# Optimization experiments

Hardware: AMD Instinct MI355X
Metric: run time of the kernel (lower is better)

Reference implementation:

```python
import jax, jax.numpy as jnp
import numpy as np

RESOLUTION = 0.1  # init arg `resolution`; hard=True -> hardtanh branch


def setup_inputs() -> dict:
    key = jax.random.key(0)
    B, L = 32, 1024  # documents x sentences per document
    score = jax.random.normal(key, (B * L,), dtype=jnp.float32)
    score_idx = jnp.arange(B * L, dtype=jnp.int32).reshape(B, L)
    return {"score": score, "score_idx": score_idx}


def _toeplitz(s):
    # Equivalent of pad_score: rows i = n-1 .. 1 of concat(zeros(n), s)
    # score_hat[r, j] = s[j - 1 - r] if j - 1 - r >= 0 else 0
    n = s.shape[0]
    r = jnp.arange(n - 1)[:, None]
    j = jnp.arange(n)[None, :]
    idx = j - 1 - r
    return jnp.where(idx >= 0, s[jnp.clip(idx, 0)], jnp.zeros((), s.dtype))


def _prob(score_hat, s):
    # hard=True: (hardtanh((hat - s)/res * 2 + 1) + 1) / 2
    z = (score_hat - s[None, :]) / RESOLUTION * 2.0 + 1.0
    return (jnp.clip(z, -1.0, 1.0) + 1.0) * 0.5


def _gate(s_doc):
    s = s_doc[1:-1]  # drop first/last sentence scores, length n = L-2
    fwd = jnp.cumprod(_prob(_toeplitz(s), s), axis=0)   # [n-1, n]
    sb = s[::-1]
    bwd = jnp.cumprod(_prob(_toeplitz(sb), sb), axis=0)  # [n-1, n]
    return jnp.stack([fwd, bwd], axis=0)  # [2, n-1, n]


def reference(score, score_idx):
    docs = score[score_idx]          # [B, L] gather per score_idx
    return jax.vmap(_gate)(docs)     # [B, 2, L-3, L-2]
```

## Files before the change

### kernel.cpp

```cpp
#include <hip/hip_runtime.h>

#define TPB     256
#define LSEQ    1024
#define NCOL    1022
#define NROW    1021
#define NPAD    1024
#define SLDS    2048
#define NCHUNK  4
#define RPC     256

typedef float v2f __attribute__((ext_vector_type(2)));
typedef float v4f __attribute__((ext_vector_type(4)));

__device__ __forceinline__ float clamp01(float x) {
    return fminf(fmaxf(x, 0.0f), 1.0f);
}

__global__ __launch_bounds__(TPB) void gate_kernel(
    const float* __restrict__ score,
    const int*   __restrict__ score_idx,
    float*       __restrict__ out)
{
    __shared__ __align__(16) float sp[SLDS];

    const int bid = blockIdx.x;
    const int ch  = bid >> 6;
    const int bd  = bid & 63;
    const int d   = bd & 1;
    const int b   = bd >> 1;
    const int tid = threadIdx.x;

    for (int i = tid; i < NPAD; i += TPB) sp[i] = 0.0f;
    if (tid < 2) sp[NPAD + NCOL + tid] = 0.0f;
    const int* idxRow = score_idx + b * LSEQ + 1;
    for (int i = tid; i < NCOL; i += TPB) {
        int src = d ? (NCOL - 1 - i) : i;
        sp[NPAD + i] = score[idxRow[src]];
    }
    __syncthreads();

    const int j = tid * 4;
    const float s0 = sp[NPAD + j    ], s1 = sp[NPAD + j + 1];
    const float s2 = sp[NPAD + j + 2], s3 = sp[NPAD + j + 3];
    const float c0 = 1.0f - 10.0f * s0, c1 = 1.0f - 10.0f * s1;
    const float c2 = 1.0f - 10.0f * s2, c3 = 1.0f - 10.0f * s3;

    float a0 = 1.0f, a1 = 1.0f, a2 = 1.0f, a3 = 1.0f;
    float C1 = s0, C2 = s1, C3 = s2;
    int   m  = NPAD + j - 1;

#define STEP(X)                                                     \
    {   float _x = (X);                                             \
        float p0 = clamp01(__builtin_fmaf(_x, 10.0f, c0));          \
        float p1 = clamp01(__builtin_fmaf(C1, 10.0f, c1));          \
        float p2 = clamp01(__builtin_fmaf(C2, 10.0f, c2));          \
        float p3 = clamp01(__builtin_fmaf(C3, 10.0f, c3));          \
        a0 *= p0; a1 *= p1; a2 *= p2; a3 *= p3;                     \
        C3 = C2; C2 = C1; C1 = _x; }

    #pragma unroll 1
    for (int bt = 0; bt < ch * (RPC / 8); ++bt) {
        v4f hi = *(const v4f*)&sp[m - 3];
        v4f lo = *(const v4f*)&sp[m - 7];
        m -= 8;
        STEP(hi.w); STEP(hi.z); STEP(hi.y); STEP(hi.x);
        STEP(lo.w); STEP(lo.z); STEP(lo.y); STEP(lo.x);
    }

    const int r0 = ch * RPC;
    const int r1 = (r0 + RPC < NROW) ? (r0 + RPC) : NROW;
    const int nrows = r1 - r0;
    const bool half = (tid == TPB - 1);

    float* outp = out + (size_t)bd * NROW * NCOL + (size_t)r0 * NCOL + j;

#define EMIT                                                        \
    {   if (half) { v2f w2; w2.x = a0; w2.y = a1;                   \
                    *(v2f*)outp = w2; }                             \
        else      { v4f w; w.x = a0; w.y = a1; w.z = a2; w.w = a3;  \
                    *(v4f*)outp = w; }                              \
        outp += NCOL; }

    #pragma unroll 1
    for (int bt = 0; bt < nrows / 8; ++bt) {
        v4f hi = *(const v4f*)&sp[m - 3];
        v4f lo = *(const v4f*)&sp[m - 7];
        m -= 8;
        STEP(hi.w); EMIT; STEP(hi.z); EMIT; STEP(hi.y); EMIT; STEP(hi.x); EMIT;
        STEP(lo.w); EMIT; STEP(lo.z); EMIT; STEP(lo.y); EMIT; STEP(lo.x); EMIT;
    }
    #pragma unroll 1
    for (int r = nrows & ~7; r < nrows; ++r) {
        float x = sp[m]; --m;
        STEP(x); EMIT;
    }
#undef STEP
#undef EMIT
}

extern "C" void kernel_launch(void* const* d_in, const int* in_sizes, int n_in,
                              void* d_out, int out_size, void* d_ws, size_t ws_size,
                              hipStream_t stream)
{
    const float* score = (const float*)d_in[0];
    const int*   sidx  = (const int*)d_in[1];
    float*       out   = (float*)d_out;

    const int B = in_sizes[0] / LSEQ;
    dim3 grid(B * 2 * NCHUNK), block(TPB);
    gate_kernel<<<grid, block, 0, stream>>>(score, sidx, out);
}
```

Before: 44.55 us.

## Split row chunks further and precompute chunk prefix products in workspace

Raises the chunk count from 4 to 8 and adds a first kernel that computes each chunk's partial cumulative product, so the store kernel combines earlier chunks' partials instead of replaying all preceding rows serially. This removes the load imbalance where later chunks spent most of their time on prefix recomputation and gives twice as many blocks for the memory-bound store phase. In exchange there is an extra kernel launch plus a small workspace write and read. If the workspace is too small, it falls back to serial recomputation.

```diff
diff --git a/kernel.cpp b/kernel.cpp
--- a/kernel.cpp
+++ b/kernel.cpp
@@ -6,8 +6,10 @@
 #define NROW    1021
 #define NPAD    1024
 #define SLDS    2048
-#define NCHUNK  4
-#define RPC     256
+#define NCHUNK  8
+#define RPC     128
+#define WS_STRIDE 1024
+#define WS_NEED  ((NCHUNK - 1) * 64 * WS_STRIDE * sizeof(float))
 
 typedef float v2f __attribute__((ext_vector_type(2)));
 typedef float v4f __attribute__((ext_vector_type(4)));
@@ -16,20 +18,8 @@
     return fminf(fmaxf(x, 0.0f), 1.0f);
 }
 
-__global__ __launch_bounds__(TPB) void gate_kernel(
-    const float* __restrict__ score,
-    const int*   __restrict__ score_idx,
-    float*       __restrict__ out)
-{
-    __shared__ __align__(16) float sp[SLDS];
-
-    const int bid = blockIdx.x;
-    const int ch  = bid >> 6;
-    const int bd  = bid & 63;
-    const int d   = bd & 1;
-    const int b   = bd >> 1;
-    const int tid = threadIdx.x;
-
+__device__ __forceinline__ void stage(float* sp, const float* score,
+                                      const int* score_idx, int b, int d, int tid) {
     for (int i = tid; i < NPAD; i += TPB) sp[i] = 0.0f;
     if (tid < 2) sp[NPAD + NCOL + tid] = 0.0f;
     const int* idxRow = score_idx + b * LSEQ + 1;
@@ -38,16 +28,7 @@
         sp[NPAD + i] = score[idxRow[src]];
     }
     __syncthreads();
-
-    const int j = tid * 4;
-    const float s0 = sp[NPAD + j    ], s1 = sp[NPAD + j + 1];
-    const float s2 = sp[NPAD + j + 2], s3 = sp[NPAD + j + 3];
-    const float c0 = 1.0f - 10.0f * s0, c1 = 1.0f - 10.0f * s1;
-    const float c2 = 1.0f - 10.0f * s2, c3 = 1.0f - 10.0f * s3;
-
-    float a0 = 1.0f, a1 = 1.0f, a2 = 1.0f, a3 = 1.0f;
-    float C1 = s0, C2 = s1, C3 = s2;
-    int   m  = NPAD + j - 1;
+}
 
 #define STEP(X)                                                     \
     {   float _x = (X);                                             \
@@ -58,25 +39,91 @@
         a0 *= p0; a1 *= p1; a2 *= p2; a3 *= p3;                     \
         C3 = C2; C2 = C1; C1 = _x; }
 
+__global__ __launch_bounds__(TPB) void gate_partial(
+    const float* __restrict__ score,
+    const int*   __restrict__ score_idx,
+    float*       __restrict__ ws)
+{
+    __shared__ __align__(16) float sp[SLDS];
+    const int bid = blockIdx.x;
+    const int c   = bid >> 6;
+    const int bd  = bid & 63;
+    stage(sp, score, score_idx, bd >> 1, bd & 1, threadIdx.x);
+
+    const int j  = threadIdx.x * 4;
+    const int r0 = c * RPC;
+    const float c0 = 1.0f - 10.0f * sp[NPAD + j    ];
+    const float c1 = 1.0f - 10.0f * sp[NPAD + j + 1];
+    const float c2 = 1.0f - 10.0f * sp[NPAD + j + 2];
+    const float c3 = 1.0f - 10.0f * sp[NPAD + j + 3];
+
+    float a0 = 1.0f, a1 = 1.0f, a2 = 1.0f, a3 = 1.0f;
+    float C1 = sp[NPAD + j - r0], C2 = sp[NPAD + j + 1 - r0], C3 = sp[NPAD + j + 2 - r0];
+    int   m  = NPAD + j - 1 - r0;
+
     #pragma unroll 1
-    for (int bt = 0; bt < ch * (RPC / 8); ++bt) {
+    for (int bt = 0; bt < RPC / 8; ++bt) {
         v4f hi = *(const v4f*)&sp[m - 3];
         v4f lo = *(const v4f*)&sp[m - 7];
         m -= 8;
         STEP(hi.w); STEP(hi.z); STEP(hi.y); STEP(hi.x);
         STEP(lo.w); STEP(lo.z); STEP(lo.y); STEP(lo.x);
     }
+    v4f P; P.x = a0; P.y = a1; P.z = a2; P.w = a3;
+    *(v4f*)&ws[(size_t)bid * WS_STRIDE + j] = P;
+}
 
-    const int r0 = ch * RPC;
-    const int r1 = (r0 + RPC < NROW) ? (r0 + RPC) : NROW;
-    const int nrows = r1 - r0;
+template <bool USE_WS>
+__global__ __launch_bounds__(TPB) void gate_store(
+    const float* __restrict__ score,
+    const int*   __restrict__ score_idx,
+    const float* __restrict__ ws,
+    float*       __restrict__ out)
+{
+    __shared__ __align__(16) float sp[SLDS];
+    const int bid = blockIdx.x;
+    const int ch  = bid >> 6;
+    const int bd  = bid & 63;
+    stage(sp, score, score_idx, bd >> 1, bd & 1, threadIdx.x);
+
+    const int tid = threadIdx.x;
+    const int j   = tid * 4;
+    const int r0  = ch * RPC;
+    const float c0 = 1.0f - 10.0f * sp[NPAD + j    ];
+    const float c1 = 1.0f - 10.0f * sp[NPAD + j + 1];
+    const float c2 = 1.0f - 10.0f * sp[NPAD + j + 2];
+    const float c3 = 1.0f - 10.0f * sp[NPAD + j + 3];
+
+    float a0 = 1.0f, a1 = 1.0f, a2 = 1.0f, a3 = 1.0f;
+    float C1, C2, C3;
+    int   m;
+
+    if (USE_WS) {
+        for (int c = 0; c < ch; ++c) {
+            v4f P = *(const v4f*)&ws[(size_t)(c * 64 + bd) * WS_STRIDE + j];
+            a0 *= P.x; a1 *= P.y; a2 *= P.z; a3 *= P.w;
+        }
+        C1 = sp[NPAD + j - r0]; C2 = sp[NPAD + j + 1 - r0]; C3 = sp[NPAD + j + 2 - r0];
+        m  = NPAD + j - 1 - r0;
+    } else {
+        C1 = sp[NPAD + j]; C2 = sp[NPAD + j + 1]; C3 = sp[NPAD + j + 2];
+        m  = NPAD + j - 1;
+        #pragma unroll 1
+        for (int bt = 0; bt < (r0 >> 3); ++bt) {
+            v4f hi = *(const v4f*)&sp[m - 3];
+            v4f lo = *(const v4f*)&sp[m - 7];
+            m -= 8;
+            STEP(hi.w); STEP(hi.z); STEP(hi.y); STEP(hi.x);
+            STEP(lo.w); STEP(lo.z); STEP(lo.y); STEP(lo.x);
+        }
+    }
+
+    const int nrows = (r0 + RPC < NROW) ? RPC : (NROW - r0);
     const bool half = (tid == TPB - 1);
-
     float* outp = out + (size_t)bd * NROW * NCOL + (size_t)r0 * NCOL + j;
 
 #define EMIT                                                        \
-    {   if (half) { v2f w2; w2.x = a0; w2.y = a1;                   \
-                    *(v2f*)outp = w2; }                             \
+    {   if (half) { v2f w2; w2.x = a0; w2.y = a1; *(v2f*)outp = w2; } \
         else      { v4f w; w.x = a0; w.y = a1; w.z = a2; w.w = a3;  \
                     *(v4f*)outp = w; }                              \
         outp += NCOL; }
@@ -94,7 +141,6 @@
         float x = sp[m]; --m;
         STEP(x); EMIT;
     }
-#undef STEP
 #undef EMIT
 }
 
@@ -105,8 +151,12 @@
     const float* score = (const float*)d_in[0];
     const int*   sidx  = (const int*)d_in[1];
     float*       out   = (float*)d_out;
+    float*       ws    = (float*)d_ws;
 
-    const int B = in_sizes[0] / LSEQ;
-    dim3 grid(B * 2 * NCHUNK), block(TPB);
-    gate_kernel<<<grid, block, 0, stream>>>(score, sidx, out);
+    if (ws_size >= WS_NEED) {
+        gate_partial<<<dim3((NCHUNK - 1) * 64), dim3(TPB), 0, stream>>>(score, sidx, ws);
+        gate_store<true><<<dim3(NCHUNK * 64), dim3(TPB), 0, stream>>>(score, sidx, ws, out);
+    } else {
+        gate_store<false><<<dim3(NCHUNK * 64), dim3(TPB), 0, stream>>>(score, sidx, ws, out);
+    }
 }
```

Measured after the change: 50.58 us. +13.5%, slower.
